# Kernel optimization log

Measured on AMD Instinct MI355X. Metric: run time of the kernel, lower is better.

## Reference

```python
import jax, jax.numpy as jnp
import numpy as np

B, C_HIGH, C_LOW, H, W = 4, 256, 128, 64, 64
HEADS = 4
HEAD_DIM = C_LOW // HEADS
FFN = 2 * C_LOW
EPS = 1e-5


def group_norm1(x, w, b):
    # GroupNorm(num_groups=1): normalize over (C,H,W) per sample, per-channel affine
    mu = jnp.mean(x, axis=(1, 2, 3), keepdims=True)
    var = jnp.var(x, axis=(1, 2, 3), keepdims=True)
    xn = (x - mu) * jax.lax.rsqrt(var + EPS)
    return xn * w[None, :, None, None] + b[None, :, None, None]


def conv1x1(x, Wm):
    # 1x1 conv, no bias: Wm [C_out, C_in], x [B,C_in,H,W]
    return jnp.einsum('oc,bchw->bohw', Wm, x)


def setup_inputs() -> dict:
    key = jax.random.key(0)
    ks = jax.random.split(key, 10)
    s = 0.05
    return {
        'high_feature': jax.random.normal(ks[0], (B, C_HIGH, H, W), jnp.float32),
        'low_feature': jax.random.normal(ks[1], (B, C_LOW, H, W), jnp.float32),
        'norm_high_w': jnp.ones((C_HIGH,), jnp.float32),
        'norm_high_b': jnp.zeros((C_HIGH,), jnp.float32),
        'norm_low_w': jnp.ones((C_LOW,), jnp.float32),
        'norm_low_b': jnp.zeros((C_LOW,), jnp.float32),
        'norm_ffn_w': jnp.ones((C_LOW,), jnp.float32),
        'norm_ffn_b': jnp.zeros((C_LOW,), jnp.float32),
        'Wq': jax.random.normal(ks[2], (C_LOW, C_HIGH), jnp.float32) * s,
        'Wk': jax.random.normal(ks[3], (C_LOW, C_LOW), jnp.float32) * s,
        'Wv': jax.random.normal(ks[4], (C_LOW, C_LOW), jnp.float32) * s,
        'Wproj': jax.random.normal(ks[5], (C_LOW, C_LOW), jnp.float32) * s,
        'Wffn1': jax.random.normal(ks[6], (FFN, C_LOW), jnp.float32) * s,
        'Wffn2': jax.random.normal(ks[7], (C_LOW, FFN), jnp.float32) * s,
        # nn.Parameter(torch.zeros(1)) in the original; use 0.1 for nontrivial grads
        'gamma_attn': jnp.full((1,), 0.1, jnp.float32),
        'gamma_ffn': jnp.full((1,), 0.1, jnp.float32),
    }


def reference(high_feature, low_feature, norm_high_w, norm_high_b, norm_low_w,
              norm_low_b, norm_ffn_w, norm_ffn_b, Wq, Wk, Wv, Wproj, Wffn1,
              Wffn2, gamma_attn, gamma_ffn):
    Bb, _, Hh, Ww = low_feature.shape
    N = Hh * Ww
    scale = HEAD_DIM ** (-0.5)

    high_norm = group_norm1(high_feature, norm_high_w, norm_high_b)
    low_norm = group_norm1(low_feature, norm_low_w, norm_low_b)

    q = conv1x1(high_norm, Wq).reshape(Bb, HEADS, HEAD_DIM, N).transpose(0, 1, 3, 2)  # [B,h,N,d]
    k = conv1x1(low_norm, Wk).reshape(Bb, HEADS, HEAD_DIM, N)                         # [B,h,d,N]
    v = conv1x1(low_norm, Wv).reshape(Bb, HEADS, HEAD_DIM, N).transpose(0, 1, 3, 2)   # [B,h,N,d]

    attn = jax.nn.softmax(jnp.einsum('bhnd,bhdm->bhnm', q, k) * scale, axis=-1)       # [B,h,N,N]
    out = jnp.einsum('bhnm,bhmd->bhnd', attn, v)                                      # [B,h,N,d]
    out = out.transpose(0, 1, 3, 2).reshape(Bb, C_LOW, Hh, Ww)
    out = conv1x1(out, Wproj)

    x = low_feature + gamma_attn[0] * out
    xn = group_norm1(x, norm_ffn_w, norm_ffn_b)
    ffn = conv1x1(jax.nn.gelu(conv1x1(xn, Wffn1), approximate=False), Wffn2)
    return x + gamma_ffn[0] * ffn
```

## Files before the change

### kernel.cpp

```cpp
#include <hip/hip_runtime.h>
#include <hip/hip_bf16.h>
#include <math.h>

#define EPS 1e-5f
#define BB 4
#define CHIGH 256
#define CLOW 128
#define NN 4096
#define NHEADS 4
#define HDIM 32
#define FFN_DIM 256
#define SPLITS 4

typedef __bf16 b8 __attribute__((ext_vector_type(8)));
typedef float f4 __attribute__((ext_vector_type(4)));

__device__ __forceinline__ unsigned int cvt_pk(float lo, float hi) {
    float2 t; t.x = lo; t.y = hi;
    __hip_bfloat162 h = __float22bfloat162_rn(t);
    unsigned int r;
    __builtin_memcpy(&r, &h, sizeof(r));
    return r;
}
__device__ __forceinline__ float b2f(unsigned short u) {
    unsigned int x = ((unsigned int)u) << 16;
    float f;
    __builtin_memcpy(&f, &x, 4);
    return f;
}
__device__ __forceinline__ float fexp2(float x) {
#if __has_builtin(__builtin_amdgcn_exp2f)
    return __builtin_amdgcn_exp2f(x);
#else
    return exp2f(x);
#endif
}

__global__ __launch_bounds__(256)
void prep_kernel(const float* __restrict__ high, const float* __restrict__ low,
                 float* __restrict__ acc,
                 const float* __restrict__ w0, const float* __restrict__ w1,
                 const float* __restrict__ w2, const float* __restrict__ w3,
                 const float* __restrict__ w4, const float* __restrict__ w5,
                 unsigned short* __restrict__ dst)
{
    const int z = blockIdx.z;
    if (z < 2) {
        const int perSample = z == 0 ? CHIGH * NN : CLOW * NN;
        const float* X = z == 0 ? high : low;
        float* ac = acc + (z == 0 ? 0 : 8);
        const int b = blockIdx.y;
        const float4* xp = (const float4*)(X + (size_t)b * perSample);
        const int n4 = perSample >> 2;
        float s = 0.f, s2 = 0.f;
        for (int i = blockIdx.x * blockDim.x + threadIdx.x; i < n4;
             i += gridDim.x * blockDim.x) {
            float4 v = xp[i];
            s  += v.x + v.y + v.z + v.w;
            s2 += v.x * v.x + v.y * v.y + v.z * v.z + v.w * v.w;
        }
        for (int off = 32; off; off >>= 1) {
            s  += __shfl_down(s, off, 64);
            s2 += __shfl_down(s2, off, 64);
        }
        __shared__ float ls[4], ls2[4];
        const int w = threadIdx.x >> 6;
        if ((threadIdx.x & 63) == 0) { ls[w] = s; ls2[w] = s2; }
        __syncthreads();
        if (threadIdx.x == 0) {
            atomicAdd(&ac[2 * b], ls[0] + ls[1] + ls[2] + ls[3]);
            atomicAdd(&ac[2 * b + 1], ls2[0] + ls2[1] + ls2[2] + ls2[3]);
        }
    } else {
        const int idx = blockIdx.y * 64 + blockIdx.x;
        const int m = idx >> 5;
        if (m >= 6) return;
        const int sizes[6] = {32768, 16384, 16384, 16384, 32768, 32768};
        const int offs[6]  = {0, 32768, 49152, 65536, 81920, 114688};
        const float* src = m == 0 ? w0 : m == 1 ? w1 : m == 2 ? w2 : m == 3 ? w3
                         : m == 4 ? w4 : w5;
        const int i = ((idx & 31) * 256 + threadIdx.x) * 4;
        if (i >= sizes[m]) return;
        float4 v = *(const float4*)&src[i];
        uint2 pk;
        pk.x = cvt_pk(v.x, v.y);
        pk.y = cvt_pk(v.z, v.w);
        *(uint2*)&dst[offs[m] + i] = pk;
    }
}

__global__ __launch_bounds__(256)
void qkv_kernel(const unsigned short* __restrict__ wbf,
                const float* __restrict__ high, const float* __restrict__ low,
                unsigned short* __restrict__ Qt, unsigned short* __restrict__ Kt,
                unsigned short* __restrict__ Vt,
                const float* __restrict__ nh_w, const float* __restrict__ nh_b,
                const float* __restrict__ nl_w, const float* __restrict__ nl_b,
                const float* __restrict__ st)
{
    __shared__ unsigned short XsRaw[32 * 264];
    const int b = blockIdx.y;
    const int n0 = blockIdx.x * 32;
    const int t = threadIdx.x;
    const int w = t >> 6, lm = t & 15, quad = (t & 63) >> 4;
    unsigned int* xw = (unsigned int*)XsRaw;

    if (blockIdx.z == 0) {
        const float invCnt = 1.0f / ((float)CHIGH * NN);
        const float mean = st[2 * b] * invCnt;
        const float rstd = rsqrtf(st[2 * b + 1] * invCnt - mean * mean + EPS);
        const float* Xb = high + (size_t)b * CHIGH * NN;
        #pragma unroll
        for (int it = 0; it < 4; it++) {
            const int s = it * 256 + t;
            const int kp = s >> 3;
            const int k2 = kp << 1;
            const int nc = (s & 7) << 2;
            const size_t ro = (size_t)k2 * NN + n0 + nc;
            float4 pa = *(const float4*)&Xb[ro];
            float4 pb = *(const float4*)&Xb[ro + NN];
            const float sc0 = nh_w[k2] * rstd,     sb0 = nh_b[k2] - mean * sc0;
            const float sc1 = nh_w[k2 + 1] * rstd, sb1 = nh_b[k2 + 1] - mean * sc1;
            pa.x = pa.x * sc0 + sb0; pa.y = pa.y * sc0 + sb0;
            pa.z = pa.z * sc0 + sb0; pa.w = pa.w * sc0 + sb0;
            pb.x = pb.x * sc1 + sb1; pb.y = pb.y * sc1 + sb1;
            pb.z = pb.z * sc1 + sb1; pb.w = pb.w * sc1 + sb1;
            xw[(nc + 0) * 132 + kp] = cvt_pk(pa.x, pb.x);
            xw[(nc + 1) * 132 + kp] = cvt_pk(pa.y, pb.y);
            xw[(nc + 2) * 132 + kp] = cvt_pk(pa.z, pb.z);
            xw[(nc + 3) * 132 + kp] = cvt_pk(pa.w, pb.w);
        }
        __syncthreads();
        const int ng = w & 1, mh = w >> 1;
        f4 acc[4];
        #pragma unroll
        for (int f = 0; f < 4; f++) acc[f] = (f4){0.f, 0.f, 0.f, 0.f};
        #pragma unroll
        for (int kc = 0; kc < CHIGH; kc += 32) {
            b8 bx = *(const b8*)&XsRaw[(ng * 16 + lm) * 264 + kc + quad * 8];
            #pragma unroll
            for (int f = 0; f < 4; f++) {
                b8 af = *(const b8*)&wbf[(size_t)(mh * 64 + f * 16 + lm) * 256 + kc + quad * 8];
                acc[f] = __builtin_amdgcn_mfma_f32_16x16x32_bf16(af, bx, acc[f], 0, 0, 0);
            }
        }
        const int n = n0 + ng * 16 + lm;
        const float oscale = 0.25503480f;
        #pragma unroll
        for (int f = 0; f < 4; f++) {
            const int mb = mh * 64 + f * 16 + quad * 4;
            const int hh = mb >> 5, ddb = mb & 31;
            uint2 pk;
            pk.x = cvt_pk(acc[f][0] * oscale, acc[f][1] * oscale);
            pk.y = cvt_pk(acc[f][2] * oscale, acc[f][3] * oscale);
            *(uint2*)&Qt[((size_t)(b * NHEADS + hh) * NN + n) * 32 + ddb] = pk;
        }
    } else {
        const unsigned short* Wb = wbf + 32768;
        const float invCnt = 1.0f / ((float)CLOW * NN);
        const float mean = st[8 + 2 * b] * invCnt;
        const float rstd = rsqrtf(st[8 + 2 * b + 1] * invCnt - mean * mean + EPS);
        const float* Xb = low + (size_t)b * CLOW * NN;
        #pragma unroll
        for (int it = 0; it < 2; it++) {
            const int s = it * 256 + t;
            const int kp = s >> 3;
            const int k2 = kp << 1;
            const int nc = (s & 7) << 2;
            const size_t ro = (size_t)k2 * NN + n0 + nc;
            float4 pa = *(const float4*)&Xb[ro];
            float4 pb = *(const float4*)&Xb[ro + NN];
            const float sc0 = nl_w[k2] * rstd,     sb0 = nl_b[k2] - mean * sc0;
            const float sc1 = nl_w[k2 + 1] * rstd, sb1 = nl_b[k2 + 1] - mean * sc1;
            pa.x = pa.x * sc0 + sb0; pa.y = pa.y * sc0 + sb0;
            pa.z = pa.z * sc0 + sb0; pa.w = pa.w * sc0 + sb0;
            pb.x = pb.x * sc1 + sb1; pb.y = pb.y * sc1 + sb1;
            pb.z = pb.z * sc1 + sb1; pb.w = pb.w * sc1 + sb1;
            xw[(nc + 0) * 68 + kp] = cvt_pk(pa.x, pb.x);
            xw[(nc + 1) * 68 + kp] = cvt_pk(pa.y, pb.y);
            xw[(nc + 2) * 68 + kp] = cvt_pk(pa.z, pb.z);
            xw[(nc + 3) * 68 + kp] = cvt_pk(pa.w, pb.w);
        }
        __syncthreads();
        f4 acc[2][4];
        #pragma unroll
        for (int ng = 0; ng < 2; ng++)
            #pragma unroll
            for (int f = 0; f < 4; f++) acc[ng][f] = (f4){0.f, 0.f, 0.f, 0.f};
        #pragma unroll
        for (int kc = 0; kc < CLOW; kc += 32) {
            b8 bx0 = *(const b8*)&XsRaw[lm * 136 + kc + quad * 8];
            b8 bx1 = *(const b8*)&XsRaw[(16 + lm) * 136 + kc + quad * 8];
            #pragma unroll
            for (int f = 0; f < 4; f++) {
                b8 af = *(const b8*)&Wb[(size_t)(w * 64 + f * 16 + lm) * 128 + kc + quad * 8];
                acc[0][f] = __builtin_amdgcn_mfma_f32_16x16x32_bf16(af, bx0, acc[0][f], 0, 0, 0);
                acc[1][f] = __builtin_amdgcn_mfma_f32_16x16x32_bf16(af, bx1, acc[1][f], 0, 0, 0);
            }
        }
        if (w < 2) {
            #pragma unroll
            for (int ng = 0; ng < 2; ng++) {
                const int n = n0 + ng * 16 + lm;
                #pragma unroll
                for (int f = 0; f < 4; f++) {
                    const int mb = w * 64 + f * 16 + quad * 4;
                    const int hh = mb >> 5, ddb = mb & 31;
                    uint2 pk;
                    pk.x = cvt_pk(acc[ng][f][0], acc[ng][f][1]);
                    pk.y = cvt_pk(acc[ng][f][2], acc[ng][f][3]);
                    *(uint2*)&Kt[((size_t)(b * NHEADS + hh) * NN + n) * 32 + ddb] = pk;
                }
            }
        } else {
            #pragma unroll
            for (int ng = 0; ng < 2; ng++) {
                const int n = n0 + ng * 16 + lm;
                const size_t nblk = ((size_t)(n >> 5) << 10) + (n & 31);
                #pragma unroll
                for (int f = 0; f < 4; f++) {
                    const int db = (w - 2) * 64 + f * 16 + quad * 4;
                    const int hh = db >> 5;
                    const size_t hb = (size_t)(b * NHEADS + hh) * NN * 32;
                    #pragma unroll
                    for (int r = 0; r < 4; r++) {
                        const int d = (db + r) & 31;
                        unsigned int u = cvt_pk(acc[ng][f][r], 0.f);
                        Vt[hb + nblk + (size_t)d * 32] = (unsigned short)(u & 0xFFFF);
                    }
                }
            }
        }
    }
}

__global__ __launch_bounds__(256)
void flash_kernel(const unsigned short* __restrict__ Qt,
                  const unsigned short* __restrict__ Kt,
                  const unsigned short* __restrict__ Vt,
                  unsigned short* __restrict__ Op, float* __restrict__ Lp)
{
    __shared__ unsigned short Ps[4][32][72];

    const int bz = blockIdx.z;
    const int b = bz >> 2, half = bz & 3;
    const int h = blockIdx.y;
    const int n0 = blockIdx.x * 128;
    const int t = threadIdx.x;
    const int w = t >> 6;
    const int lm = t & 15, quad = (t & 63) >> 4;

    const unsigned short* Qh = Qt + (size_t)(b * NHEADS + h) * NN * 32;
    const unsigned short* Kh = Kt + (size_t)(b * NHEADS + h) * NN * 32;
    const unsigned short* Vh = Vt + (size_t)(b * NHEADS + h) * NN * 32;

    b8 aq[2];
    aq[0] = *(const b8*)&Qh[(size_t)(n0 + w * 32 + lm) * 32 + quad * 8];
    aq[1] = *(const b8*)&Qh[(size_t)(n0 + w * 32 + 16 + lm) * 32 + quad * 8];

    b8 ones;
    #pragma unroll
    for (int j = 0; j < 8; j++) ones[j] = (__bf16)1.0f;

    f4 ocT[2][2];
    f4 lsum[2];
    #pragma unroll
    for (int u = 0; u < 2; u++) {
        lsum[u] = (f4){0.f, 0.f, 0.f, 0.f};
        ocT[0][u] = (f4){0.f, 0.f, 0.f, 0.f};
        ocT[1][u] = (f4){0.f, 0.f, 0.f, 0.f};
    }

    const int m_lo = half * (NN / SPLITS), m_hi = m_lo + NN / SPLITS;
    for (int m0 = m_lo; m0 < m_hi; m0 += 64) {
        b8 bk[4], av[2][2];
        #pragma unroll
        for (int f = 0; f < 4; f++)
            bk[f] = *(const b8*)&Kh[(size_t)(m0 + f * 16 + lm) * 32 + quad * 8];
        #pragma unroll
        for (int c = 0; c < 2; c++) {
            const size_t vb = (size_t)(m0 + c * 32) * 32 + quad * 8;
            av[0][c] = *(const b8*)&Vh[vb + (size_t)lm * 32];
            av[1][c] = *(const b8*)&Vh[vb + (size_t)(16 + lm) * 32];
        }

        f4 st[4][2];
        #pragma unroll
        for (int f = 0; f < 4; f++)
            #pragma unroll
            for (int u = 0; u < 2; u++) {
                f4 z = {0.f, 0.f, 0.f, 0.f};
                st[f][u] = __builtin_amdgcn_mfma_f32_16x16x32_bf16(bk[f], aq[u], z, 0, 0, 0);
            }

        #pragma unroll
        for (int f = 0; f < 4; f++)
            #pragma unroll
            for (int u = 0; u < 2; u++) {
                float e0 = fexp2(st[f][u][0]);
                float e1 = fexp2(st[f][u][1]);
                float e2 = fexp2(st[f][u][2]);
                float e3 = fexp2(st[f][u][3]);
                uint2 pk;
                pk.x = cvt_pk(e0, e1);
                pk.y = cvt_pk(e2, e3);
                *(uint2*)&Ps[w][u * 16 + lm][f * 16 + quad * 4] = pk;
            }

        #pragma unroll
        for (int c = 0; c < 2; c++)
            #pragma unroll
            for (int u = 0; u < 2; u++) {
                b8 bp = *(const b8*)&Ps[w][u * 16 + lm][c * 32 + quad * 8];
                ocT[0][u] = __builtin_amdgcn_mfma_f32_16x16x32_bf16(av[0][c], bp, ocT[0][u], 0, 0, 0);
                ocT[1][u] = __builtin_amdgcn_mfma_f32_16x16x32_bf16(av[1][c], bp, ocT[1][u], 0, 0, 0);
                lsum[u]   = __builtin_amdgcn_mfma_f32_16x16x32_bf16(ones, bp, lsum[u], 0, 0, 0);
            }
    }

    unsigned short* OpB = Op + ((size_t)(half * BB + b) * CLOW + h * HDIM) * NN;
    float* LpB = Lp + ((size_t)(half * BB + b) * NHEADS + h) * NN;
    #pragma unroll
    for (int u = 0; u < 2; u++) {
        const int n = n0 + w * 32 + u * 16 + lm;
        if (quad == 0) LpB[n] = lsum[u][0];
        #pragma unroll
        for (int hh = 0; hh < 2; hh++)
            #pragma unroll
            for (int r = 0; r < 4; r++) {
                const int d = hh * 16 + quad * 4 + r;
                unsigned int uu = cvt_pk(ocT[hh][u][r], 0.f);
                OpB[(size_t)d * NN + n] = (unsigned short)(uu & 0xFFFF);
            }
    }
}

__global__ __launch_bounds__(256)
void proj_kernel(const unsigned short* __restrict__ Wb,
                 const unsigned short* __restrict__ Opart, const float* __restrict__ Lp,
                 const float* __restrict__ low, float* __restrict__ Xout,
                 const float* __restrict__ gp, float* __restrict__ stOut)
{
    __shared__ unsigned short Xs[32][136];
    __shared__ float red[8];
    const int b = blockIdx.z;
    const int mblk = blockIdx.y;
    const int n0 = blockIdx.x * 32;
    const int t = threadIdx.x;
    const int w = t >> 6, lm = t & 15, quad = (t & 63) >> 4;
    const int ng = w & 1, mh = w >> 1;
    unsigned int* xw = (unsigned int*)&Xs[0][0];

    #pragma unroll
    for (int it = 0; it < 2; it++) {
        const int s = it * 256 + t;
        const int kp = s >> 3;
        const int k2 = kp << 1;
        const int nc = (s & 7) << 2;
        const size_t ro = (size_t)k2 * NN + n0 + nc;
        const int hh = k2 >> 5;
        const size_t lo = (size_t)(b * NHEADS + hh) * NN + n0 + nc;
        float4 l4 = *(const float4*)&Lp[lo];
        #pragma unroll
        for (int sp = 1; sp < SPLITS; sp++)
            l4 += *(const float4*)&Lp[lo + (size_t)sp * BB * NHEADS * NN];
        float4 pa = {0.f, 0.f, 0.f, 0.f}, pb = {0.f, 0.f, 0.f, 0.f};
        #pragma unroll
        for (int sp = 0; sp < SPLITS; sp++) {
            const unsigned short* Os = Opart + (size_t)sp * BB * CLOW * NN
                                     + (size_t)b * CLOW * NN + ro;
            ushort4 ua = *(const ushort4*)Os;
            ushort4 ub = *(const ushort4*)(Os + NN);
            pa.x += b2f(ua.x); pa.y += b2f(ua.y); pa.z += b2f(ua.z); pa.w += b2f(ua.w);
            pb.x += b2f(ub.x); pb.y += b2f(ub.y); pb.z += b2f(ub.z); pb.w += b2f(ub.w);
        }
        float4 iv;
        iv.x = 1.f / l4.x; iv.y = 1.f / l4.y; iv.z = 1.f / l4.z; iv.w = 1.f / l4.w;
        pa.x *= iv.x; pa.y *= iv.y; pa.z *= iv.z; pa.w *= iv.w;
        pb.x *= iv.x; pb.y *= iv.y; pb.z *= iv.z; pb.w *= iv.w;
        xw[(nc + 0) * 68 + kp] = cvt_pk(pa.x, pb.x);
        xw[(nc + 1) * 68 + kp] = cvt_pk(pa.y, pb.y);
        xw[(nc + 2) * 68 + kp] = cvt_pk(pa.z, pb.z);
        xw[(nc + 3) * 68 + kp] = cvt_pk(pa.w, pb.w);
    }
    __syncthreads();

    f4 acc[2];
    acc[0] = (f4){0.f, 0.f, 0.f, 0.f};
    acc[1] = (f4){0.f, 0.f, 0.f, 0.f};
    #pragma unroll
    for (int kc = 0; kc < CLOW; kc += 32) {
        b8 bx = *(const b8*)&Xs[ng * 16 + lm][kc + quad * 8];
        #pragma unroll
        for (int f = 0; f < 2; f++) {
            b8 af = *(const b8*)&Wb[(size_t)(mblk * 64 + mh * 32 + f * 16 + lm) * 128
                                    + kc + quad * 8];
            acc[f] = __builtin_amdgcn_mfma_f32_16x16x32_bf16(af, bx, acc[f], 0, 0, 0);
        }
    }

    const float g = gp[0];
    const float* Rb = low + (size_t)b * CLOW * NN;
    float* Yb = Xout + (size_t)b * CLOW * NN;
    const int n = n0 + ng * 16 + lm;
    float s = 0.f, s2 = 0.f;
    #pragma unroll
    for (int f = 0; f < 2; f++)
        #pragma unroll
        for (int r = 0; r < 4; r++) {
            const int m = mblk * 64 + mh * 32 + f * 16 + quad * 4 + r;
            const size_t off = (size_t)m * NN + n;
            float v = Rb[off] + g * acc[f][r];
            Yb[off] = v;
            s += v; s2 += v * v;
        }
    for (int off = 32; off; off >>= 1) {
        s  += __shfl_down(s, off, 64);
        s2 += __shfl_down(s2, off, 64);
    }
    if ((t & 63) == 0) { red[w] = s; red[4 + w] = s2; }
    __syncthreads();
    if (t == 0) {
        atomicAdd(&stOut[2 * b], red[0] + red[1] + red[2] + red[3]);
        atomicAdd(&stOut[2 * b + 1], red[4] + red[5] + red[6] + red[7]);
    }
}

__global__ __launch_bounds__(512)
void ffn_kernel(const unsigned short* __restrict__ W1, const unsigned short* __restrict__ W2,
                const float* __restrict__ X, float* __restrict__ Out,
                const float* __restrict__ nw, const float* __restrict__ nb,
                const float* __restrict__ st, const float* __restrict__ gp)
{
    __shared__ unsigned short Xs[32][136];
    __shared__ unsigned short Hs[32][264];
    const int b = blockIdx.y;
    const int n0 = blockIdx.x * 32;
    const int t = threadIdx.x;
    const int w = t >> 6, lm = t & 15, quad = (t & 63) >> 4;

    const float invCnt = 1.0f / ((float)CLOW * NN);
    const float mean = st[2 * b] * invCnt;
    const float rstd = rsqrtf(st[2 * b + 1] * invCnt - mean * mean + EPS);

    const float* Xb = X + (size_t)b * CLOW * NN;
    unsigned int* xw = (unsigned int*)&Xs[0][0];
    {
        const int s = t;
        const int kp = s >> 3;
        const int k2 = kp << 1;
        const int nc = (s & 7) << 2;
        const size_t ro = (size_t)k2 * NN + n0 + nc;
        float4 pa = *(const float4*)&Xb[ro];
        float4 pb = *(const float4*)&Xb[ro + NN];
        const float sc0 = nw[k2] * rstd,     sb0 = nb[k2] - mean * sc0;
        const float sc1 = nw[k2 + 1] * rstd, sb1 = nb[k2 + 1] - mean * sc1;
        pa.x = pa.x * sc0 + sb0; pa.y = pa.y * sc0 + sb0;
        pa.z = pa.z * sc0 + sb0; pa.w = pa.w * sc0 + sb0;
        pb.x = pb.x * sc1 + sb1; pb.y = pb.y * sc1 + sb1;
        pb.z = pb.z * sc1 + sb1; pb.w = pb.w * sc1 + sb1;
        xw[(nc + 0) * 68 + kp] = cvt_pk(pa.x, pb.x);
        xw[(nc + 1) * 68 + kp] = cvt_pk(pa.y, pb.y);
        xw[(nc + 2) * 68 + kp] = cvt_pk(pa.z, pb.z);
        xw[(nc + 3) * 68 + kp] = cvt_pk(pa.w, pb.w);
    }
    __syncthreads();

    f4 hv[2][2];
    #pragma unroll
    for (int ng = 0; ng < 2; ng++) {
        hv[ng][0] = (f4){0.f, 0.f, 0.f, 0.f};
        hv[ng][1] = (f4){0.f, 0.f, 0.f, 0.f};
    }
    #pragma unroll
    for (int kc = 0; kc < CLOW; kc += 32) {
        b8 bx0 = *(const b8*)&Xs[lm][kc + quad * 8];
        b8 bx1 = *(const b8*)&Xs[16 + lm][kc + quad * 8];
        #pragma unroll
        for (int f = 0; f < 2; f++) {
            b8 af = *(const b8*)&W1[(size_t)(w * 32 + f * 16 + lm) * 128 + kc + quad * 8];
            hv[0][f] = __builtin_amdgcn_mfma_f32_16x16x32_bf16(af, bx0, hv[0][f], 0, 0, 0);
            hv[1][f] = __builtin_amdgcn_mfma_f32_16x16x32_bf16(af, bx1, hv[1][f], 0, 0, 0);
        }
    }
    #pragma unroll
    for (int ng = 0; ng < 2; ng++)
        #pragma unroll
        for (int f = 0; f < 2; f++) {
            float g0 = hv[ng][f][0], g1 = hv[ng][f][1];
            float g2 = hv[ng][f][2], g3 = hv[ng][f][3];
            g0 = 0.5f * g0 * (1.f + erff(g0 * 0.70710678118654752f));
            g1 = 0.5f * g1 * (1.f + erff(g1 * 0.70710678118654752f));
            g2 = 0.5f * g2 * (1.f + erff(g2 * 0.70710678118654752f));
            g3 = 0.5f * g3 * (1.f + erff(g3 * 0.70710678118654752f));
            uint2 pk;
            pk.x = cvt_pk(g0, g1);
            pk.y = cvt_pk(g2, g3);
            *(uint2*)&Hs[ng * 16 + lm][w * 32 + f * 16 + quad * 4] = pk;
        }
    __syncthreads();

    f4 o[2];
    o[0] = (f4){0.f, 0.f, 0.f, 0.f};
    o[1] = (f4){0.f, 0.f, 0.f, 0.f};
    #pragma unroll
    for (int kc = 0; kc < FFN_DIM; kc += 32) {
        b8 bh0 = *(const b8*)&Hs[lm][kc + quad * 8];
        b8 bh1 = *(const b8*)&Hs[16 + lm][kc + quad * 8];
        b8 af = *(const b8*)&W2[(size_t)(w * 16 + lm) * 256 + kc + quad * 8];
        o[0] = __builtin_amdgcn_mfma_f32_16x16x32_bf16(af, bh0, o[0], 0, 0, 0);
        o[1] = __builtin_amdgcn_mfma_f32_16x16x32_bf16(af, bh1, o[1], 0, 0, 0);
    }
    const float g = gp[0];
    float* Ob = Out + (size_t)b * CLOW * NN;
    #pragma unroll
    for (int ng = 0; ng < 2; ng++) {
        const int n = n0 + ng * 16 + lm;
        #pragma unroll
        for (int r = 0; r < 4; r++) {
            const int m = w * 16 + quad * 4 + r;
            const size_t off = (size_t)m * NN + n;
            Ob[off] = Xb[off] + g * o[ng][r];
        }
    }
}

extern "C" void kernel_launch(void* const* d_in, const int* in_sizes, int n_in,
                              void* d_out, int out_size, void* d_ws, size_t ws_size,
                              hipStream_t stream)
{
    const float* high  = (const float*)d_in[0];
    const float* low   = (const float*)d_in[1];
    const float* nh_w  = (const float*)d_in[2];
    const float* nh_b  = (const float*)d_in[3];
    const float* nl_w  = (const float*)d_in[4];
    const float* nl_b  = (const float*)d_in[5];
    const float* nf_w  = (const float*)d_in[6];
    const float* nf_b  = (const float*)d_in[7];
    const float* Wq    = (const float*)d_in[8];
    const float* Wk    = (const float*)d_in[9];
    const float* Wv    = (const float*)d_in[10];
    const float* Wproj = (const float*)d_in[11];
    const float* Wff1  = (const float*)d_in[12];
    const float* Wff2  = (const float*)d_in[13];
    const float* g_at  = (const float*)d_in[14];
    const float* g_ff  = (const float*)d_in[15];
    float* out = (float*)d_out;

    float* ws    = (float*)d_ws;
    float* stats = ws;
    unsigned short* wbf = (unsigned short*)(ws + 64);
    unsigned short* qt = wbf + 147456;
    unsigned short* kt = qt + (size_t)BB * NHEADS * NN * 32;
    unsigned short* vt = kt + (size_t)BB * NHEADS * NN * 32;
    unsigned short* opart = vt + (size_t)BB * CLOW * NN;
    float* lpart = (float*)(opart + (size_t)SPLITS * BB * CLOW * NN);
    float* x     = lpart + (size_t)SPLITS * BB * NHEADS * NN;

    (void)hipMemsetAsync(stats, 0, 64 * sizeof(float), stream);

    prep_kernel<<<dim3(64, BB, 3), 256, 0, stream>>>(high, low, stats,
                                                     Wq, Wk, Wv, Wproj, Wff1, Wff2, wbf);

    qkv_kernel<<<dim3(128, BB, 2), 256, 0, stream>>>(wbf, high, low, qt, kt, vt,
                                                     nh_w, nh_b, nl_w, nl_b, stats);

    flash_kernel<<<dim3(NN / 128, NHEADS, BB * SPLITS), 256, 0, stream>>>(qt, kt, vt,
                                                                          opart, lpart);

    proj_kernel<<<dim3(128, 2, BB), 256, 0, stream>>>(wbf + 65536, opart, lpart,
                                                      low, x, g_at, stats + 16);

    ffn_kernel<<<dim3(128, BB), 512, 0, stream>>>(wbf + 81920, wbf + 114688, x, out,
                                                  nf_w, nf_b, stats + 16, g_ff);
}
```

Before: 239.8 us.

## Pre-tile bf16 weights into MFMA fragment order and double-buffer attention K/V loads

The weight conversion kernel now writes each bf16 weight matrix in 16x32 tiles laid out in MFMA fragment order. Each wave's A-fragment load then reads one contiguous 1KB chunk instead of strided rows, which is meant to improve coalescing in the QKV, projection and FFN GEMMs. Separately, the attention inner loop is restructured with two fragment buffers so the K/V loads for the next 64-key tile are issued before the current tile is computed. This adds register pressure and assumes the number of tiles per split is even.

```diff
diff --git a/kernel.cpp b/kernel.cpp
--- a/kernel.cpp
+++ b/kernel.cpp
@@ -77,15 +77,21 @@
         if (m >= 6) return;
         const int sizes[6] = {32768, 16384, 16384, 16384, 32768, 32768};
         const int offs[6]  = {0, 32768, 49152, 65536, 81920, 114688};
+        const int Ks[6]    = {256, 128, 128, 128, 128, 256};
         const float* src = m == 0 ? w0 : m == 1 ? w1 : m == 2 ? w2 : m == 3 ? w3
                          : m == 4 ? w4 : w5;
         const int i = ((idx & 31) * 256 + threadIdx.x) * 4;
         if (i >= sizes[m]) return;
+        const int K = Ks[m];
+        const int row = i / K, col = i % K;
+        const int mt = row >> 4, mr = row & 15;
+        const int kt = col >> 5, kr = col & 31;
         float4 v = *(const float4*)&src[i];
         uint2 pk;
         pk.x = cvt_pk(v.x, v.y);
         pk.y = cvt_pk(v.z, v.w);
-        *(uint2*)&dst[offs[m] + i] = pk;
+        const int doff = offs[m] + (((mt * (K >> 5)) + kt) << 9) + (mr << 5) + kr;
+        *(uint2*)&dst[doff] = pk;
     }
 }
 
@@ -103,6 +109,7 @@
     const int n0 = blockIdx.x * 32;
     const int t = threadIdx.x;
     const int w = t >> 6, lm = t & 15, quad = (t & 63) >> 4;
+    const int fo = lm * 32 + quad * 8;
     unsigned int* xw = (unsigned int*)XsRaw;
 
     if (blockIdx.z == 0) {
@@ -136,11 +143,11 @@
         #pragma unroll
         for (int f = 0; f < 4; f++) acc[f] = (f4){0.f, 0.f, 0.f, 0.f};
         #pragma unroll
-        for (int kc = 0; kc < CHIGH; kc += 32) {
-            b8 bx = *(const b8*)&XsRaw[(ng * 16 + lm) * 264 + kc + quad * 8];
+        for (int kc = 0; kc < 8; kc++) {
+            b8 bx = *(const b8*)&XsRaw[(ng * 16 + lm) * 264 + kc * 32 + quad * 8];
             #pragma unroll
             for (int f = 0; f < 4; f++) {
-                b8 af = *(const b8*)&wbf[(size_t)(mh * 64 + f * 16 + lm) * 256 + kc + quad * 8];
+                b8 af = *(const b8*)&wbf[(((mh * 4 + f) * 8 + kc) << 9) + fo];
                 acc[f] = __builtin_amdgcn_mfma_f32_16x16x32_bf16(af, bx, acc[f], 0, 0, 0);
             }
         }
@@ -188,12 +195,12 @@
             #pragma unroll
             for (int f = 0; f < 4; f++) acc[ng][f] = (f4){0.f, 0.f, 0.f, 0.f};
         #pragma unroll
-        for (int kc = 0; kc < CLOW; kc += 32) {
-            b8 bx0 = *(const b8*)&XsRaw[lm * 136 + kc + quad * 8];
-            b8 bx1 = *(const b8*)&XsRaw[(16 + lm) * 136 + kc + quad * 8];
+        for (int kc = 0; kc < 4; kc++) {
+            b8 bx0 = *(const b8*)&XsRaw[lm * 136 + kc * 32 + quad * 8];
+            b8 bx1 = *(const b8*)&XsRaw[(16 + lm) * 136 + kc * 32 + quad * 8];
             #pragma unroll
             for (int f = 0; f < 4; f++) {
-                b8 af = *(const b8*)&Wb[(size_t)(w * 64 + f * 16 + lm) * 128 + kc + quad * 8];
+                b8 af = *(const b8*)&Wb[(((w * 4 + f) * 4 + kc) << 9) + fo];
                 acc[0][f] = __builtin_amdgcn_mfma_f32_16x16x32_bf16(af, bx0, acc[0][f], 0, 0, 0);
                 acc[1][f] = __builtin_amdgcn_mfma_f32_16x16x32_bf16(af, bx1, acc[1][f], 0, 0, 0);
             }
@@ -271,9 +278,7 @@
         ocT[1][u] = (f4){0.f, 0.f, 0.f, 0.f};
     }
 
-    const int m_lo = half * (NN / SPLITS), m_hi = m_lo + NN / SPLITS;
-    for (int m0 = m_lo; m0 < m_hi; m0 += 64) {
-        b8 bk[4], av[2][2];
+    auto loadFrags = [&](int m0, b8* bk, b8 (*av)[2]) {
         #pragma unroll
         for (int f = 0; f < 4; f++)
             bk[f] = *(const b8*)&Kh[(size_t)(m0 + f * 16 + lm) * 32 + quad * 8];
@@ -283,30 +288,21 @@
             av[0][c] = *(const b8*)&Vh[vb + (size_t)lm * 32];
             av[1][c] = *(const b8*)&Vh[vb + (size_t)(16 + lm) * 32];
         }
-
-        f4 st[4][2];
-        #pragma unroll
-        for (int f = 0; f < 4; f++)
+    };
+
+    auto computeTile = [&](const b8* bk, const b8 (*av)[2]) {
+        #pragma unroll
+        for (int f = 0; f < 4; f++) {
             #pragma unroll
             for (int u = 0; u < 2; u++) {
                 f4 z = {0.f, 0.f, 0.f, 0.f};
-                st[f][u] = __builtin_amdgcn_mfma_f32_16x16x32_bf16(bk[f], aq[u], z, 0, 0, 0);
-            }
-
-        #pragma unroll
-        for (int f = 0; f < 4; f++)
-            #pragma unroll
-            for (int u = 0; u < 2; u++) {
-                float e0 = fexp2(st[f][u][0]);
-                float e1 = fexp2(st[f][u][1]);
-                float e2 = fexp2(st[f][u][2]);
-                float e3 = fexp2(st[f][u][3]);
+                f4 sv = __builtin_amdgcn_mfma_f32_16x16x32_bf16(bk[f], aq[u], z, 0, 0, 0);
                 uint2 pk;
-                pk.x = cvt_pk(e0, e1);
-                pk.y = cvt_pk(e2, e3);
+                pk.x = cvt_pk(fexp2(sv[0]), fexp2(sv[1]));
+                pk.y = cvt_pk(fexp2(sv[2]), fexp2(sv[3]));
                 *(uint2*)&Ps[w][u * 16 + lm][f * 16 + quad * 4] = pk;
             }
-
+        }
         #pragma unroll
         for (int c = 0; c < 2; c++)
             #pragma unroll
@@ -316,6 +312,20 @@
                 ocT[1][u] = __builtin_amdgcn_mfma_f32_16x16x32_bf16(av[1][c], bp, ocT[1][u], 0, 0, 0);
                 lsum[u]   = __builtin_amdgcn_mfma_f32_16x16x32_bf16(ones, bp, lsum[u], 0, 0, 0);
             }
+    };
+
+    const int m_lo = half * (NN / SPLITS);
+    constexpr int nT = NN / SPLITS / 64;
+    b8 bkA[4], bkB[4];
+    b8 avA[2][2], avB[2][2];
+    loadFrags(m_lo, bkA, avA);
+    #pragma unroll 1
+    for (int it = 0; it < nT; it += 2) {
+        loadFrags(m_lo + (it + 1) * 64, bkB, avB);
+        computeTile(bkA, avA);
+        const int m0n = (it + 2 < nT) ? m_lo + (it + 2) * 64 : m_lo;
+        loadFrags(m0n, bkA, avA);
+        computeTile(bkB, avB);
     }
 
     unsigned short* OpB = Op + ((size_t)(half * BB + b) * CLOW + h * HDIM) * NN;
@@ -349,6 +359,7 @@
     const int t = threadIdx.x;
     const int w = t >> 6, lm = t & 15, quad = (t & 63) >> 4;
     const int ng = w & 1, mh = w >> 1;
+    const int fo = lm * 32 + quad * 8;
     unsigned int* xw = (unsigned int*)&Xs[0][0];
 
     #pragma unroll
@@ -389,12 +400,12 @@
     acc[0] = (f4){0.f, 0.f, 0.f, 0.f};
     acc[1] = (f4){0.f, 0.f, 0.f, 0.f};
     #pragma unroll
-    for (int kc = 0; kc < CLOW; kc += 32) {
-        b8 bx = *(const b8*)&Xs[ng * 16 + lm][kc + quad * 8];
+    for (int kc = 0; kc < 4; kc++) {
+        b8 bx = *(const b8*)&Xs[ng * 16 + lm][kc * 32 + quad * 8];
         #pragma unroll
         for (int f = 0; f < 2; f++) {
-            b8 af = *(const b8*)&Wb[(size_t)(mblk * 64 + mh * 32 + f * 16 + lm) * 128
-                                    + kc + quad * 8];
+            const int mt = mblk * 4 + mh * 2 + f;
+            b8 af = *(const b8*)&Wb[((mt * 4 + kc) << 9) + fo];
             acc[f] = __builtin_amdgcn_mfma_f32_16x16x32_bf16(af, bx, acc[f], 0, 0, 0);
         }
     }
@@ -438,6 +449,7 @@
     const int n0 = blockIdx.x * 32;
     const int t = threadIdx.x;
     const int w = t >> 6, lm = t & 15, quad = (t & 63) >> 4;
+    const int fo = lm * 32 + quad * 8;
 
     const float invCnt = 1.0f / ((float)CLOW * NN);
     const float mean = st[2 * b] * invCnt;
@@ -473,12 +485,13 @@
         hv[ng][1] = (f4){0.f, 0.f, 0.f, 0.f};
     }
     #pragma unroll
-    for (int kc = 0; kc < CLOW; kc += 32) {
-        b8 bx0 = *(const b8*)&Xs[lm][kc + quad * 8];
-        b8 bx1 = *(const b8*)&Xs[16 + lm][kc + quad * 8];
+    for (int kc = 0; kc < 4; kc++) {
+        b8 bx0 = *(const b8*)&Xs[lm][kc * 32 + quad * 8];
+        b8 bx1 = *(const b8*)&Xs[16 + lm][kc * 32 + quad * 8];
         #pragma unroll
         for (int f = 0; f < 2; f++) {
-            b8 af = *(const b8*)&W1[(size_t)(w * 32 + f * 16 + lm) * 128 + kc + quad * 8];
+            const int mt = w * 2 + f;
+            b8 af = *(const b8*)&W1[((mt * 4 + kc) << 9) + fo];
             hv[0][f] = __builtin_amdgcn_mfma_f32_16x16x32_bf16(af, bx0, hv[0][f], 0, 0, 0);
             hv[1][f] = __builtin_amdgcn_mfma_f32_16x16x32_bf16(af, bx1, hv[1][f], 0, 0, 0);
         }
@@ -504,10 +517,10 @@
     o[0] = (f4){0.f, 0.f, 0.f, 0.f};
     o[1] = (f4){0.f, 0.f, 0.f, 0.f};
     #pragma unroll
-    for (int kc = 0; kc < FFN_DIM; kc += 32) {
-        b8 bh0 = *(const b8*)&Hs[lm][kc + quad * 8];
-        b8 bh1 = *(const b8*)&Hs[16 + lm][kc + quad * 8];
-        b8 af = *(const b8*)&W2[(size_t)(w * 16 + lm) * 256 + kc + quad * 8];
+    for (int kc = 0; kc < 8; kc++) {
+        b8 bh0 = *(const b8*)&Hs[lm][kc * 32 + quad * 8];
+        b8 bh1 = *(const b8*)&Hs[16 + lm][kc * 32 + quad * 8];
+        b8 af = *(const b8*)&W2[((w * 8 + kc) << 9) + fo];
         o[0] = __builtin_amdgcn_mfma_f32_16x16x32_bf16(af, bh0, o[0], 0, 0, 0);
         o[1] = __builtin_amdgcn_mfma_f32_16x16x32_bf16(af, bh1, o[1], 0, 0, 0);
     }
```

Result: no change. 236.6 us (-1.4%).
